# Kernel optimization log

Measured on AMD Instinct MI355X. Metric: run time of the kernel, lower is better.

## Reference

```python
import jax, jax.numpy as jnp
import numpy as np

B, S, DIM, HD = 4, 1024, 2048, 128
H = DIM // HD  # 16 heads
GN_EPS = 1e-3  # Keras GroupNormalization default epsilon


def setup_inputs() -> dict:
    key = jax.random.key(0)
    ks = jax.random.split(key, 8)
    x = jax.random.normal(ks[0], (B, S, DIM), dtype=jnp.float32)
    k = jax.random.normal(ks[1], (B, S, DIM), dtype=jnp.float32)
    v = jax.random.normal(ks[2], (B, S, DIM), dtype=jnp.float32)
    # One shared QKV projection weight per head (dict.fromkeys bug in source
    # makes Q, K, V use the SAME Dense layer). Keras Dense: y = x @ W, W:(in,out)
    Wh = jax.random.normal(ks[3], (H, HD, HD), dtype=jnp.float32) / np.sqrt(HD)
    wg_w = jax.random.normal(ks[4], (DIM, DIM), dtype=jnp.float32) / np.sqrt(DIM)
    wo_w = jax.random.normal(ks[5], (DIM, DIM), dtype=jnp.float32) / np.sqrt(DIM)
    gn_gamma = jnp.ones((DIM,), dtype=jnp.float32)
    gn_beta = jnp.zeros((DIM,), dtype=jnp.float32)
    return {"x": x, "k": k, "v": v, "Wh": Wh, "wg_w": wg_w, "wo_w": wo_w,
            "gn_gamma": gn_gamma, "gn_beta": gn_beta}


def _decay_masks(n_heads, seq_len):
    # Source: band_part(gamma**(i-j), 0, -1) then transpose ->
    # D[h, i, j] = gamma_h ** (j - i) for j <= i, else 0.
    gam = 1.0 - 2.0 ** (-5.0 - jnp.arange(n_heads, dtype=jnp.float32))  # (H,)
    idx = jnp.arange(seq_len, dtype=jnp.float32)
    expo = idx[None, :] - idx[:, None]               # (S,S): j - i
    D = jnp.where(expo[None, :, :] <= 0,
                  gam[:, None, None] ** expo[None, :, :], 0.0)  # (H,S,S)
    # TF: D /= reduce_sum(D, 1)**0.5 broadcasts row-sums along the COLUMN axis
    return D / jnp.sqrt(D.sum(axis=-1))[:, None, :]


def reference(x, k, v, Wh, wg_w, wo_w, gn_gamma, gn_beta):
    b, s, dim = x.shape
    h, hd, _ = Wh.shape
    # split last axis into contiguous per-head chunks
    xh = x.reshape(b, s, h, hd)
    kh = k.reshape(b, s, h, hd)
    vh = v.reshape(b, s, h, hd)
    # Q, K, V share the same per-head weight (faithful to dict.fromkeys)
    Q = jnp.einsum('bshd,hde->bshe', xh, Wh)
    K = jnp.einsum('bshd,hde->bshe', kh, Wh)
    V = jnp.einsum('bshd,hde->bshe', vh, Wh)
    scores = jnp.einsum('bshe,bthe->bhst', Q, K) / jnp.sqrt(jnp.float32(hd))
    Dn = _decay_masks(h, s)                          # (H,S,S)
    masked = scores * Dn[None, :, :, :]              # (B,H,S,S)
    # source reduces over axis 0 == BATCH, then abs, then clamp at 1
    A = jnp.maximum(jnp.abs(masked.sum(axis=0)), 1.0)  # (H,S,S)
    O = jnp.einsum('hst,bthe->bshe', A, V).reshape(b, s, dim)
    # GroupNormalization(groups=1): per-token layernorm over channels
    mu = O.mean(axis=-1, keepdims=True)
    var = O.var(axis=-1, keepdims=True)
    Y = (O - mu) / jnp.sqrt(var + GN_EPS) * gn_gamma + gn_beta
    W = jax.nn.relu(x @ wg_w)                        # gated branch
    return (W * Y) @ wo_w
```

## Files before the change

kernel.cpp:

```cpp
#include <hip/hip_runtime.h>
#include <math.h>

constexpr int Bc = 4, Sc = 1024, Dc = 2048, HDc = 128, Hc = 16;
constexpr int BSc = Bc * Sc;
constexpr int KQKc = Bc * HDc;
#define GN_EPS 1e-3f

typedef __bf16 bf16x8 __attribute__((ext_vector_type(8)));
typedef __bf16 bf16x4 __attribute__((ext_vector_type(4)));
typedef float f32x4 __attribute__((ext_vector_type(4)));

constexpr size_t OFF_Q   = 0;
constexpr size_t OFF_K   = OFF_Q + (size_t)Hc * Sc * KQKc / 2;
constexpr size_t OFF_VB  = OFF_K + (size_t)Hc * Sc * KQKc / 2;
constexpr size_t OFF_VT  = OFF_VB + (size_t)BSc * Dc / 2;
constexpr size_t OFF_A   = OFF_VT + (size_t)BSc * Dc / 2;
constexpr size_t OFF_O   = OFF_A + (size_t)Hc * Sc * Sc / 2;
constexpr size_t OFF_CT  = OFF_O + (size_t)BSc * Dc;
constexpr size_t OFF_PN  = OFF_CT + (size_t)Hc * Sc;
constexpr size_t OFF_XB  = OFF_PN + (size_t)Hc * Sc;
constexpr size_t OFF_WGT = OFF_XB + (size_t)BSc * Dc / 2;
constexpr size_t OFF_WOT = OFF_WGT + (size_t)Dc * Dc / 2;
constexpr size_t OFF_SUF = OFF_WOT + (size_t)Dc * Dc / 2;
constexpr size_t OFF_T   = OFF_SUF + (size_t)64 * 9 * HDc;
constexpr size_t OFF_WHT = OFF_T + (size_t)64 * 8 * HDc;
constexpr size_t OFF_KB2 = OFF_A;
constexpr size_t OFF_VB2 = OFF_A + (size_t)BSc * Dc / 2;

#define GLOAD_LDS16(gp, lp)                                               \
  __builtin_amdgcn_global_load_lds(                                       \
      (const __attribute__((address_space(1))) void*)(gp),                \
      (__attribute__((address_space(3))) void*)(lp), 16, 0, 0)


__global__ __launch_bounds__(256) void k_tables(float* __restrict__ ct,
                                                float* __restrict__ pn) {
  int idx = blockIdx.x * 256 + threadIdx.x;
  int h = idx >> 10, t = idx & 1023;
  double gamma = 1.0 - exp2(-(double)(5 + h));
  double l2g = log2(gamma);
  double r = 1.0 / gamma;
  double rowsum = (exp2(-(double)(t + 1) * l2g) - 1.0) / (r - 1.0);
  ct[idx] = (float)(exp2((double)t * l2g) / sqrt(rowsum));
  pn[idx] = (float)exp2(-(double)t * l2g);
}

__global__ __launch_bounds__(256) void k_cast83(const float* __restrict__ s0,
                                                const float* __restrict__ s1,
                                                const float* __restrict__ s2,
                                                __bf16* __restrict__ d0,
                                                __bf16* __restrict__ d1,
                                                __bf16* __restrict__ d2) {
  const int y = blockIdx.y;
  const float* src = (y == 0) ? s0 : (y == 1) ? s1 : s2;
  __bf16* dst = (y == 0) ? d0 : (y == 1) ? d1 : d2;
  size_t i = ((size_t)blockIdx.x * 256 + threadIdx.x) * 8;
  float4 a = *(const float4*)(src + i);
  float4 b = *(const float4*)(src + i + 4);
  bf16x8 o;
  o[0] = (__bf16)a.x; o[1] = (__bf16)a.y; o[2] = (__bf16)a.z; o[3] = (__bf16)a.w;
  o[4] = (__bf16)b.x; o[5] = (__bf16)b.y; o[6] = (__bf16)b.z; o[7] = (__bf16)b.w;
  *(bf16x8*)(dst + i) = o;
}

__global__ __launch_bounds__(256) void k_castT(const float* __restrict__ src,
                                               __bf16* __restrict__ dst) {
  __shared__ float t[32][33];
  const int bx = blockIdx.x, by = blockIdx.y;
  const int tid = threadIdx.x;
  const int lx = tid & 31, ly = tid >> 5;
  #pragma unroll
  for (int r = 0; r < 32; r += 8)
    t[ly + r][lx] = src[(size_t)(by * 32 + ly + r) * Dc + bx * 32 + lx];
  __syncthreads();
  #pragma unroll
  for (int r = 0; r < 32; r += 8)
    dst[(size_t)(bx * 32 + ly + r) * Dc + by * 32 + lx] = (__bf16)t[lx][ly + r];
}

__global__ __launch_bounds__(256) void k_whT(const float* __restrict__ Wh,
                                             __bf16* __restrict__ WhT) {
  __shared__ float t[32][33];
  const int h = blockIdx.z;
  const int d0 = blockIdx.x * 32, e0 = blockIdx.y * 32;
  const int tid = threadIdx.x;
  const int lx = tid & 31, ly = tid >> 5;
  #pragma unroll
  for (int r = 0; r < 32; r += 8)
    t[ly + r][lx] = Wh[(size_t)h * HDc * HDc + (d0 + ly + r) * HDc + e0 + lx];
  __syncthreads();
  #pragma unroll
  for (int r = 0; r < 32; r += 8)
    WhT[(size_t)h * HDc * HDc + (e0 + ly + r) * HDc + d0 + lx] =
        (__bf16)t[lx][ly + r];
}

__global__ __launch_bounds__(512) void k_projm(const __bf16* __restrict__ Xb,
                                               const __bf16* __restrict__ Kb2,
                                               const __bf16* __restrict__ Vb2,
                                               const __bf16* __restrict__ WhT,
                                               __bf16* __restrict__ Qo,
                                               __bf16* __restrict__ Ko,
                                               __bf16* __restrict__ Vo) {
  const int r0 = blockIdx.x * 128;
  const int h = blockIdx.y;
  const int z = blockIdx.z;
  const __bf16* src = (z == 0) ? Xb : (z == 1) ? Kb2 : Vb2;
  __shared__ __bf16 As[128 * 32];
  __shared__ __bf16 Bs[128 * 32];
  const int tid = threadIdx.x;
  const int wave = tid >> 6, lane = tid & 63;
  const int wm = (wave >> 2) * 64, wn = (wave & 3) * 32;
  const int grow = wave * 16 + (lane >> 2);
  const int gkb = ((lane & 3) ^ ((lane >> 3) & 3)) * 8;
  const int rl = lane & 15, kq = lane >> 4;
  const int sw8 = (kq ^ ((rl >> 1) & 3)) * 8;
  const int cha = wm >> 4, chb = wn >> 4;
  const __bf16* wb = WhT + (size_t)h * HDc * HDc;
  f32x4 acc[4][2] = {{}};
  for (int k0 = 0; k0 < HDc; k0 += 32) {
    GLOAD_LDS16(src + (size_t)(r0 + grow) * Dc + h * HDc + k0 + gkb,
                As + wave * 512);
    GLOAD_LDS16(wb + (size_t)grow * HDc + k0 + gkb, Bs + wave * 512);
    __syncthreads();
    bf16x8 a[4], b[2];
    #pragma unroll
    for (int i = 0; i < 4; ++i)
      a[i] = *(const bf16x8*)&As[(cha + i) * 512 + rl * 32 + sw8];
    #pragma unroll
    for (int j = 0; j < 2; ++j)
      b[j] = *(const bf16x8*)&Bs[(chb + j) * 512 + rl * 32 + sw8];
    #pragma unroll
    for (int i = 0; i < 4; ++i)
      #pragma unroll
      for (int j = 0; j < 2; ++j)
        acc[i][j] = __builtin_amdgcn_mfma_f32_16x16x32_bf16(a[i], b[j],
                                                            acc[i][j], 0, 0, 0);
    __syncthreads();
  }
  #pragma unroll
  for (int i = 0; i < 4; ++i) {
    #pragma unroll
    for (int j = 0; j < 2; ++j) {
      const int col = wn + j * 16 + rl;
      #pragma unroll
      for (int r = 0; r < 4; ++r) {
        const int row = r0 + wm + i * 16 + kq * 4 + r;
        const __bf16 v = (__bf16)acc[i][j][r];
        if (z == 2) {
          Vo[(size_t)row * Dc + h * HDc + col] = v;
        } else {
          const int s = row & 1023, bb = row >> 10;
          __bf16* dst = (z == 0) ? Qo : Ko;
          dst[((size_t)(h * Sc + s) * Bc + bb) * HDc + col] = v;
        }
      }
    }
  }
}

__global__ __launch_bounds__(256) void k_vt(const __bf16* __restrict__ VB,
                                            __bf16* __restrict__ Vt) {
  __shared__ float tl[32][33];
  const int bh = blockIdx.z, bb = bh >> 4, h = bh & 15;
  const int t0 = blockIdx.x * 32, e0 = blockIdx.y * 32;
  const int tid = threadIdx.x;
  const int lx = tid & 31, ly = tid >> 5;
  #pragma unroll
  for (int r = 0; r < 32; r += 8)
    tl[ly + r][lx] =
        (float)VB[(size_t)(bb * Sc + t0 + ly + r) * Dc + h * HDc + e0 + lx];
  __syncthreads();
  #pragma unroll
  for (int r = 0; r < 32; r += 8)
    Vt[((size_t)bh * HDc + e0 + ly + r) * Sc + t0 + lx] = (__bf16)tl[lx][ly + r];
}

__global__ __launch_bounds__(256) void k_vsum(const __bf16* __restrict__ VB,
                                              float* __restrict__ T) {
  const int jj = blockIdx.x, bh = blockIdx.y;
  const int bb = bh >> 4, h = bh & 15;
  const int tid = threadIdx.x;
  const int tp = tid >> 7, e = tid & 127;
  const __bf16* base =
      VB + (size_t)(bb * Sc + jj * 128 + tp * 64) * Dc + h * HDc + e;
  float a0 = 0.f, a1 = 0.f, a2 = 0.f, a3 = 0.f;
  float a4 = 0.f, a5 = 0.f, a6 = 0.f, a7 = 0.f;
  for (int t = 0; t < 64; t += 8) {
    a0 += (float)base[(size_t)(t + 0) * Dc];
    a1 += (float)base[(size_t)(t + 1) * Dc];
    a2 += (float)base[(size_t)(t + 2) * Dc];
    a3 += (float)base[(size_t)(t + 3) * Dc];
    a4 += (float)base[(size_t)(t + 4) * Dc];
    a5 += (float)base[(size_t)(t + 5) * Dc];
    a6 += (float)base[(size_t)(t + 6) * Dc];
    a7 += (float)base[(size_t)(t + 7) * Dc];
  }
  const float s = ((a0 + a1) + (a2 + a3)) + ((a4 + a5) + (a6 + a7));
  __shared__ float red[2][128];
  red[tp][e] = s;
  __syncthreads();
  if (tp == 0)
    T[((size_t)bh * 8 + jj) * HDc + e] = red[0][e] + red[1][e];
}

__global__ __launch_bounds__(128) void k_vscan(const float* __restrict__ T,
                                               float* __restrict__ SufV) {
  const int bh = blockIdx.x;
  const int e = threadIdx.x;
  float acc = 0.f;
  SufV[((size_t)bh * 9 + 8) * HDc + e] = 0.f;
  for (int jj = 7; jj >= 1; --jj) {
    acc += T[((size_t)bh * 8 + jj) * HDc + e];
    SufV[((size_t)bh * 9 + jj) * HDc + e] = acc;
  }
}

__global__ __launch_bounds__(512) void k_ssm(const __bf16* __restrict__ Q,
                                             const __bf16* __restrict__ Kb,
                                             const float* __restrict__ ct,
                                             const float* __restrict__ pn,
                                             __bf16* __restrict__ A) {
  const int bx = blockIdx.x, by = blockIdx.y;
  if (bx > by) return;
  const int h = blockIdx.z;
  const int t0 = bx * 128, s0 = by * 128;
  const int tid = threadIdx.x;
  __bf16* Ah = A + (size_t)h * Sc * Sc;
  __shared__ __bf16 Qs[128 * 32];
  __shared__ __bf16 Ks[128 * 32];
  const int wave = tid >> 6, lane = tid & 63;
  const int wm = (wave >> 2) * 64, wn = (wave & 3) * 32;
  const int grow = wave * 16 + (lane >> 2);
  const int gkb = ((lane & 3) ^ ((lane >> 3) & 3)) * 8;
  const int rl = lane & 15, kq = lane >> 4;
  const int sw8 = (kq ^ ((rl >> 1) & 3)) * 8;
  const int cha = wm >> 4, chb = wn >> 4;
  f32x4 acc[4][2] = {{}};
  const __bf16* qbase = Q + (size_t)(h * Sc + s0) * KQKc;
  const __bf16* kbase = Kb + (size_t)(h * Sc + t0) * KQKc;
  for (int k0 = 0; k0 < KQKc; k0 += 32) {
    GLOAD_LDS16(qbase + (size_t)grow * KQKc + k0 + gkb, Qs + wave * 512);
    GLOAD_LDS16(kbase + (size_t)grow * KQKc + k0 + gkb, Ks + wave * 512);
    __syncthreads();
    bf16x8 a[4], b[2];
    #pragma unroll
    for (int i = 0; i < 4; ++i)
      a[i] = *(const bf16x8*)&Qs[(cha + i) * 512 + rl * 32 + sw8];
    #pragma unroll
    for (int j = 0; j < 2; ++j)
      b[j] = *(const bf16x8*)&Ks[(chb + j) * 512 + rl * 32 + sw8];
    #pragma unroll
    for (int i = 0; i < 4; ++i)
      #pragma unroll
      for (int j = 0; j < 2; ++j)
        acc[i][j] = __builtin_amdgcn_mfma_f32_16x16x32_bf16(a[i], b[j],
                                                            acc[i][j], 0, 0, 0);
    __syncthreads();
  }
  const float rs = 0.088388347648318447f;
  #pragma unroll
  for (int i = 0; i < 4; ++i) {
    #pragma unroll
    for (int j = 0; j < 2; ++j) {
      const int t = t0 + wn + j * 16 + rl;
      const float ctv = ct[h * Sc + t] * rs;
      #pragma unroll
      for (int r = 0; r < 4; ++r) {
        const int s = s0 + wm + i * 16 + kq * 4 + r;
        float v = 1.0f;
        if (t <= s) v = fmaxf(fabsf(ctv * pn[h * Sc + s] * acc[i][j][r]), 1.0f);
        Ah[(size_t)s * Sc + t] = (__bf16)v;
      }
    }
  }
}

__global__ __launch_bounds__(512) void k_avm(const __bf16* __restrict__ A,
                                             const __bf16* __restrict__ Vt,
                                             const float* __restrict__ SufV,
                                             float* __restrict__ O) {
  const int bh = blockIdx.z, bb = bh >> 4, h = bh & 15;
  const int itile = blockIdx.x;
  const int s0 = itile * 128;
  const int tid = threadIdx.x;
  __shared__ __bf16 As[128 * 32];
  __shared__ __bf16 Bs[128 * 32];
  const int wave = tid >> 6, lane = tid & 63;
  const int wm = (wave >> 2) * 64, wn = (wave & 3) * 32;
  const int grow = wave * 16 + (lane >> 2);
  const int gkb = ((lane & 3) ^ ((lane >> 3) & 3)) * 8;
  const int rl = lane & 15, kq = lane >> 4;
  const int sw8 = (kq ^ ((rl >> 1) & 3)) * 8;
  const int cha = wm >> 4, chb = wn >> 4;
  f32x4 acc[4][2] = {{}};
  const __bf16* abase = A + (size_t)(h * Sc + s0) * Sc;
  const __bf16* vbase = Vt + (size_t)bh * HDc * Sc;
  const int kmax = (itile + 1) * 128;
  for (int k0 = 0; k0 < kmax; k0 += 32) {
    GLOAD_LDS16(abase + (size_t)grow * Sc + k0 + gkb, As + wave * 512);
    GLOAD_LDS16(vbase + (size_t)grow * Sc + k0 + gkb, Bs + wave * 512);
    __syncthreads();
    bf16x8 a[4], b[2];
    #pragma unroll
    for (int i = 0; i < 4; ++i)
      a[i] = *(const bf16x8*)&As[(cha + i) * 512 + rl * 32 + sw8];
    #pragma unroll
    for (int j = 0; j < 2; ++j)
      b[j] = *(const bf16x8*)&Bs[(chb + j) * 512 + rl * 32 + sw8];
    #pragma unroll
    for (int i = 0; i < 4; ++i)
      #pragma unroll
      for (int j = 0; j < 2; ++j)
        acc[i][j] = __builtin_amdgcn_mfma_f32_16x16x32_bf16(a[i], b[j],
                                                            acc[i][j], 0, 0, 0);
    __syncthreads();
  }
  const float* sufr = SufV + ((size_t)bh * 9 + (itile + 1)) * HDc;
  #pragma unroll
  for (int i = 0; i < 4; ++i) {
    #pragma unroll
    for (int j = 0; j < 2; ++j) {
      const int e = wn + j * 16 + rl;
      const float sv = sufr[e];
      #pragma unroll
      for (int r = 0; r < 4; ++r) {
        const int s = s0 + wm + i * 16 + kq * 4 + r;
        O[(size_t)(bb * Sc + s) * Dc + h * HDc + e] = acc[i][j][r] + sv;
      }
    }
  }
}

__global__ __launch_bounds__(256) void k_gnorm(float* __restrict__ O,
                                               const float* __restrict__ gw,
                                               const float* __restrict__ bw) {
  const int r = blockIdx.x;
  const int tid = threadIdx.x;
  float* row = O + (size_t)r * Dc;
  const int c = tid * 4;
  float4 v0 = *(const float4*)(row + c);
  float4 v1 = *(const float4*)(row + c + 1024);
  __shared__ float red[256];
  __shared__ float sh_mu, sh_inv;
  red[tid] = v0.x + v0.y + v0.z + v0.w + v1.x + v1.y + v1.z + v1.w;
  __syncthreads();
  for (int st = 128; st > 0; st >>= 1) {
    if (tid < st) red[tid] += red[tid + st];
    __syncthreads();
  }
  if (tid == 0) sh_mu = red[0] * (1.0f / Dc);
  __syncthreads();
  const float mu = sh_mu;
  float d[8] = {v0.x - mu, v0.y - mu, v0.z - mu, v0.w - mu,
                v1.x - mu, v1.y - mu, v1.z - mu, v1.w - mu};
  float ssq = 0.f;
  #pragma unroll
  for (int i = 0; i < 8; ++i) ssq += d[i] * d[i];
  red[tid] = ssq;
  __syncthreads();
  for (int st = 128; st > 0; st >>= 1) {
    if (tid < st) red[tid] += red[tid + st];
    __syncthreads();
  }
  if (tid == 0) sh_inv = rsqrtf(red[0] * (1.0f / Dc) + GN_EPS);
  __syncthreads();
  const float inv = sh_inv;
  float4 g0 = *(const float4*)(gw + c), g1 = *(const float4*)(gw + c + 1024);
  float4 b0 = *(const float4*)(bw + c), b1 = *(const float4*)(bw + c + 1024);
  float4 o0, o1;
  o0.x = d[0] * inv * g0.x + b0.x; o0.y = d[1] * inv * g0.y + b0.y;
  o0.z = d[2] * inv * g0.z + b0.z; o0.w = d[3] * inv * g0.w + b0.w;
  o1.x = d[4] * inv * g1.x + b1.x; o1.y = d[5] * inv * g1.y + b1.y;
  o1.z = d[6] * inv * g1.z + b1.z; o1.w = d[7] * inv * g1.w + b1.w;
  *(float4*)(row + c) = o0;
  *(float4*)(row + c + 1024) = o1;
}

constexpr int NTK = Dc / 64;
constexpr int ABUFE = 128 * 64;
constexpr int BBUFE = 128 * 64;
constexpr int MG_LDS = (3 * ABUFE + 2 * BBUFE) * 2;

__global__ __launch_bounds__(256, 2) void k_mgemm(const __bf16* __restrict__ Ab,
                                                  const __bf16* __restrict__ Bt,
                                                  const float* __restrict__ Y,
                                                  __bf16* __restrict__ Gout,
                                                  float* __restrict__ Fout,
                                                  int mode) {
  extern __shared__ __bf16 lds[];
  __bf16* As = lds;
  __bf16* Bs = lds + 3 * ABUFE;
  int wid = blockIdx.y * gridDim.x + blockIdx.x;
  wid = (wid & 7) * 64 + (wid >> 3);
  const int r0 = (wid >> 4) * 128;
  const int c0 = (wid & 15) * 128;
  const int tid = threadIdx.x;
  const int wave = tid >> 6, lane = tid & 63;
  const int wr = wave >> 1, wc = wave & 1;
  const int lr = lane >> 2;
  const int lkx = ((lane & 3) ^ ((lane >> 3) & 3)) * 8;
  const int rl = lane & 15, kq = lane >> 4;
  const int swo = rl * 32 + ((kq ^ ((rl >> 1) & 3)) * 8);
  f32x4 acc[4][4] = {{}};

#define STAGE_A_(i, kt, bsel) do {                                          \
    const int ci_ = (i) * 4 + wave;                                         \
    GLOAD_LDS16(Ab + (size_t)(r0 + (ci_ >> 1) * 16 + lr) * Dc               \
                    + (kt) * 64 + (ci_ & 1) * 32 + lkx,                     \
                As + (bsel) * ABUFE + ci_ * 512);                           \
  } while (0)
#define STAGE_B_(j, kt, bsel) do {                                          \
    const int ci_ = (j) * 4 + wave;                                         \
    GLOAD_LDS16(Bt + (size_t)(c0 + (ci_ >> 1) * 16 + lr) * Dc               \
                    + (kt) * 64 + (ci_ & 1) * 32 + lkx,                     \
                Bs + (bsel) * BBUFE + ci_ * 512);                           \
  } while (0)

  STAGE_A_(0, 0, 0); STAGE_A_(1, 0, 0); STAGE_A_(2, 0, 0); STAGE_A_(3, 0, 0);
  STAGE_B_(0, 0, 0); STAGE_B_(1, 0, 0); STAGE_B_(2, 0, 0); STAGE_B_(3, 0, 0);
  STAGE_A_(0, 1, 1); STAGE_A_(1, 1, 1); STAGE_A_(2, 1, 1); STAGE_A_(3, 1, 1);
  __builtin_amdgcn_sched_barrier(0);
  asm volatile("s_waitcnt vmcnt(4)" ::: "memory");
  __builtin_amdgcn_sched_barrier(0);
  __builtin_amdgcn_s_barrier();

  int cbA = 0;
  for (int t = 0; t < NTK; ++t) {
    const int sbA = (cbA + 2 >= 3) ? cbA - 1 : cbA + 2;
    const __bf16* Ac = As + cbA * ABUFE;
    const __bf16* Bc = Bs + (t & 1) * BBUFE;
    bf16x8 a[4][2], b[4][2];
    #pragma unroll
    for (int m = 0; m < 2; ++m)
      #pragma unroll
      for (int kc = 0; kc < 2; ++kc)
        a[m][kc] = *(const bf16x8*)&Ac[((wr * 4 + m) * 2 + kc) * 512 + swo];
    #pragma unroll
    for (int n = 0; n < 2; ++n)
      #pragma unroll
      for (int kc = 0; kc < 2; ++kc)
        b[n][kc] = *(const bf16x8*)&Bc[((wc * 4 + n) * 2 + kc) * 512 + swo];
    #pragma unroll
    for (int m = 2; m < 4; ++m)
      #pragma unroll
      for (int kc = 0; kc < 2; ++kc)
        a[m][kc] = *(const bf16x8*)&Ac[((wr * 4 + m) * 2 + kc) * 512 + swo];
    #pragma unroll
    for (int n = 2; n < 4; ++n)
      #pragma unroll
      for (int kc = 0; kc < 2; ++kc)
        b[n][kc] = *(const bf16x8*)&Bc[((wc * 4 + n) * 2 + kc) * 512 + swo];
    if (t + 1 < NTK) {
      STAGE_B_(0, t + 1, (t + 1) & 1); STAGE_B_(1, t + 1, (t + 1) & 1);
      STAGE_B_(2, t + 1, (t + 1) & 1); STAGE_B_(3, t + 1, (t + 1) & 1);
    }
    if (t + 2 < NTK) {
      STAGE_A_(0, t + 2, sbA); STAGE_A_(1, t + 2, sbA);
      STAGE_A_(2, t + 2, sbA); STAGE_A_(3, t + 2, sbA);
    }
    __builtin_amdgcn_sched_barrier(0);
    __builtin_amdgcn_s_setprio(1);
    #pragma unroll
    for (int kc = 0; kc < 2; ++kc)
      #pragma unroll
      for (int m = 0; m < 2; ++m)
        #pragma unroll
        for (int n = 0; n < 2; ++n)
          acc[m][n] = __builtin_amdgcn_mfma_f32_16x16x32_bf16(
              a[m][kc], b[n][kc], acc[m][n], 0, 0, 0);
    __builtin_amdgcn_s_setprio(0);
    __builtin_amdgcn_sched_barrier(0);
    __builtin_amdgcn_s_setprio(1);
    #pragma unroll
    for (int kc = 0; kc < 2; ++kc)
      #pragma unroll
      for (int m = 2; m < 4; ++m)
        #pragma unroll
        for (int n = 0; n < 2; ++n)
          acc[m][n] = __builtin_amdgcn_mfma_f32_16x16x32_bf16(
              a[m][kc], b[n][kc], acc[m][n], 0, 0, 0);
    __builtin_amdgcn_s_setprio(0);
    __builtin_amdgcn_sched_barrier(0);
    __builtin_amdgcn_s_setprio(1);
    #pragma unroll
    for (int kc = 0; kc < 2; ++kc)
      #pragma unroll
      for (int m = 0; m < 2; ++m)
        #pragma unroll
        for (int n = 2; n < 4; ++n)
          acc[m][n] = __builtin_amdgcn_mfma_f32_16x16x32_bf16(
              a[m][kc], b[n][kc], acc[m][n], 0, 0, 0);
    __builtin_amdgcn_s_setprio(0);
    __builtin_amdgcn_sched_barrier(0);
    __builtin_amdgcn_s_setprio(1);
    #pragma unroll
    for (int kc = 0; kc < 2; ++kc)
      #pragma unroll
      for (int m = 2; m < 4; ++m)
        #pragma unroll
        for (int n = 2; n < 4; ++n)
          acc[m][n] = __builtin_amdgcn_mfma_f32_16x16x32_bf16(
              a[m][kc], b[n][kc], acc[m][n], 0, 0, 0);
    __builtin_amdgcn_s_setprio(0);
    __builtin_amdgcn_sched_barrier(0);
    asm volatile("s_waitcnt lgkmcnt(0)" ::: "memory");
    __builtin_amdgcn_sched_barrier(0);
    if (t + 2 < NTK)
      asm volatile("s_waitcnt vmcnt(4)" ::: "memory");
    else if (t + 1 < NTK)
      asm volatile("s_waitcnt vmcnt(0)" ::: "memory");
    __builtin_amdgcn_sched_barrier(0);
    __builtin_amdgcn_s_barrier();
    cbA = (cbA + 1 >= 3) ? 0 : cbA + 1;
  }
#undef STAGE_A_
#undef STAGE_B_

  #pragma unroll
  for (int mi = 0; mi < 4; ++mi) {
    #pragma unroll
    for (int nj = 0; nj < 4; ++nj) {
      const int col = c0 + wc * 64 + nj * 16 + rl;
      #pragma unroll
      for (int r = 0; r < 4; ++r) {
        const int row = r0 + wr * 64 + mi * 16 + kq * 4 + r;
        const size_t idx = (size_t)row * Dc + col;
        float v = acc[mi][nj][r];
        if (mode == 0) {
          v = fmaxf(v, 0.f) * Y[idx];
          Gout[idx] = (__bf16)v;
        } else {
          Fout[idx] = v;
        }
      }
    }
  }
}

extern "C" void kernel_launch(void* const* d_in, const int* in_sizes, int n_in,
                              void* d_out, int out_size, void* d_ws, size_t ws_size,
                              hipStream_t stream) {
  const float* x  = (const float*)d_in[0];
  const float* k  = (const float*)d_in[1];
  const float* v  = (const float*)d_in[2];
  const float* Wh = (const float*)d_in[3];
  const float* wg = (const float*)d_in[4];
  const float* wo = (const float*)d_in[5];
  const float* gg = (const float*)d_in[6];
  const float* gb = (const float*)d_in[7];
  float* ws = (float*)d_ws;
  __bf16* Q   = (__bf16*)(ws + OFF_Q);
  __bf16* Kp  = (__bf16*)(ws + OFF_K);
  __bf16* VB  = (__bf16*)(ws + OFF_VB);
  __bf16* Vt  = (__bf16*)(ws + OFF_VT);
  __bf16* A   = (__bf16*)(ws + OFF_A);
  float*  O   = ws + OFF_O;
  float*  CT  = ws + OFF_CT;
  float*  PN  = ws + OFF_PN;
  __bf16* XB  = (__bf16*)(ws + OFF_XB);
  __bf16* WGT = (__bf16*)(ws + OFF_WGT);
  __bf16* WOT = (__bf16*)(ws + OFF_WOT);
  float*  SUF = ws + OFF_SUF;
  float*  TP  = ws + OFF_T;
  __bf16* WHT = (__bf16*)(ws + OFF_WHT);
  __bf16* KB2 = (__bf16*)(ws + OFF_KB2);
  __bf16* VB2 = (__bf16*)(ws + OFF_VB2);
  __bf16* G   = (__bf16*)(ws + OFF_Q);

  static bool attr_done = false;
  if (!attr_done) {
    (void)hipFuncSetAttribute((const void*)k_mgemm,
                              hipFuncAttributeMaxDynamicSharedMemorySize,
                              MG_LDS);
    attr_done = true;
  }

  k_tables<<<Hc * Sc / 256, 256, 0, stream>>>(CT, PN);
  k_cast83<<<dim3((BSc * Dc) / (256 * 8), 3), 256, 0, stream>>>(
      x, k, v, XB, KB2, VB2);
  k_castT<<<dim3(Dc / 32, Dc / 32), 256, 0, stream>>>(wg, WGT);
  k_castT<<<dim3(Dc / 32, Dc / 32), 256, 0, stream>>>(wo, WOT);
  k_whT<<<dim3(4, 4, Hc), 256, 0, stream>>>(Wh, WHT);
  k_projm<<<dim3(BSc / 128, Hc, 3), 512, 0, stream>>>(XB, KB2, VB2, WHT,
                                                      Q, Kp, VB);
  k_vt<<<dim3(Sc / 32, HDc / 32, Bc * Hc), 256, 0, stream>>>(VB, Vt);
  k_vsum<<<dim3(8, Bc * Hc), 256, 0, stream>>>(VB, TP);
  k_vscan<<<Bc * Hc, 128, 0, stream>>>(TP, SUF);
  k_ssm<<<dim3(Sc / 128, Sc / 128, Hc), 512, 0, stream>>>(Q, Kp, CT, PN, A);
  k_avm<<<dim3(Sc / 128, 1, Bc * Hc), 512, 0, stream>>>(A, Vt, SUF, O);
  k_gnorm<<<BSc, 256, 0, stream>>>(O, gg, gb);
  k_mgemm<<<dim3(16, 32), 256, MG_LDS, stream>>>(XB, WGT, O, G, nullptr, 0);
  k_mgemm<<<dim3(16, 32), 256, MG_LDS, stream>>>(G, WOT, nullptr, nullptr,
                                                 (float*)d_out, 1);
}
```

Before: 379.6 us.

## Share pipelined 128x128 MFMA mainloop across projection, score and AV kernels

Pulls the triple/double-buffered, software-pipelined MFMA loop out of the gate/output GEMM into a reusable template. The QKV projection, masked score and A·V kernels now use it in place of their simple single-buffered loops that synced twice per k-step. Those kernels drop from 512 to 256 threads, with each wave owning a 64x64 tile. Global-to-LDS loads now overlap MFMA work, at the cost of more dynamic LDS per block and possibly lower occupancy.

```diff
diff --git a/kernel.cpp b/kernel.cpp
--- a/kernel.cpp
+++ b/kernel.cpp
@@ -33,6 +33,137 @@
       (__attribute__((address_space(3))) void*)(lp), 16, 0, 0)
 
 
+constexpr int ABUFE = 128 * 64;
+constexpr int BBUFE = 128 * 64;
+constexpr int MG_LDS = (3 * ABUFE + 2 * BBUFE) * 2;
+
+template <int ASTR, int BSTR>
+__device__ __forceinline__ void mfma_loop128(const __bf16* __restrict__ Abase,
+                                             const __bf16* __restrict__ Bbase,
+                                             const int ntk,
+                                             __bf16* As, __bf16* Bs,
+                                             const int wave, const int lane,
+                                             f32x4 acc[4][4]) {
+  const int wr = wave >> 1, wc = wave & 1;
+  const int lr = lane >> 2;
+  const int lkx = ((lane & 3) ^ ((lane >> 3) & 3)) * 8;
+  const int rl = lane & 15, kq = lane >> 4;
+  const int swo = rl * 32 + ((kq ^ ((rl >> 1) & 3)) * 8);
+
+#define SA_(i, kt, bsel) do {                                               \
+    const int ci_ = (i) * 4 + wave;                                         \
+    GLOAD_LDS16(Abase + (size_t)((ci_ >> 1) * 16 + lr) * ASTR               \
+                    + (kt) * 64 + (ci_ & 1) * 32 + lkx,                     \
+                As + (bsel) * ABUFE + ci_ * 512);                           \
+  } while (0)
+#define SB_(j, kt, bsel) do {                                               \
+    const int ci_ = (j) * 4 + wave;                                         \
+    GLOAD_LDS16(Bbase + (size_t)((ci_ >> 1) * 16 + lr) * BSTR               \
+                    + (kt) * 64 + (ci_ & 1) * 32 + lkx,                     \
+                Bs + (bsel) * BBUFE + ci_ * 512);                           \
+  } while (0)
+
+  SA_(0, 0, 0); SA_(1, 0, 0); SA_(2, 0, 0); SA_(3, 0, 0);
+  SB_(0, 0, 0); SB_(1, 0, 0); SB_(2, 0, 0); SB_(3, 0, 0);
+  SA_(0, 1, 1); SA_(1, 1, 1); SA_(2, 1, 1); SA_(3, 1, 1);
+  __builtin_amdgcn_sched_barrier(0);
+  asm volatile("s_waitcnt vmcnt(4)" ::: "memory");
+  __builtin_amdgcn_sched_barrier(0);
+  __builtin_amdgcn_s_barrier();
+
+  int cbA = 0;
+  for (int t = 0; t < ntk; ++t) {
+    const int sbA = (cbA + 2 >= 3) ? cbA - 1 : cbA + 2;
+    const __bf16* Ac = As + cbA * ABUFE;
+    const __bf16* Bc = Bs + (t & 1) * BBUFE;
+    bf16x8 a[4][2], b[4][2];
+    #pragma unroll
+    for (int m = 0; m < 2; ++m)
+      #pragma unroll
+      for (int kc = 0; kc < 2; ++kc)
+        a[m][kc] = *(const bf16x8*)&Ac[((wr * 4 + m) * 2 + kc) * 512 + swo];
+    #pragma unroll
+    for (int n = 0; n < 2; ++n)
+      #pragma unroll
+      for (int kc = 0; kc < 2; ++kc)
+        b[n][kc] = *(const bf16x8*)&Bc[((wc * 4 + n) * 2 + kc) * 512 + swo];
+    #pragma unroll
+    for (int m = 2; m < 4; ++m)
+      #pragma unroll
+      for (int kc = 0; kc < 2; ++kc)
+        a[m][kc] = *(const bf16x8*)&Ac[((wr * 4 + m) * 2 + kc) * 512 + swo];
+    #pragma unroll
+    for (int n = 2; n < 4; ++n)
+      #pragma unroll
+      for (int kc = 0; kc < 2; ++kc)
+        b[n][kc] = *(const bf16x8*)&Bc[((wc * 4 + n) * 2 + kc) * 512 + swo];
+    if (t + 1 < ntk) {
+      SB_(0, t + 1, (t + 1) & 1); SB_(1, t + 1, (t + 1) & 1);
+      SB_(2, t + 1, (t + 1) & 1); SB_(3, t + 1, (t + 1) & 1);
+    }
+    if (t + 2 < ntk) {
+      SA_(0, t + 2, sbA); SA_(1, t + 2, sbA);
+      SA_(2, t + 2, sbA); SA_(3, t + 2, sbA);
+    }
+    __builtin_amdgcn_sched_barrier(0);
+    __builtin_amdgcn_s_setprio(1);
+    #pragma unroll
+    for (int kc = 0; kc < 2; ++kc)
+      #pragma unroll
+      for (int m = 0; m < 2; ++m)
+        #pragma unroll
+        for (int n = 0; n < 2; ++n)
+          acc[m][n] = __builtin_amdgcn_mfma_f32_16x16x32_bf16(
+              a[m][kc], b[n][kc], acc[m][n], 0, 0, 0);
+    __builtin_amdgcn_s_setprio(0);
+    __builtin_amdgcn_sched_barrier(0);
+    __builtin_amdgcn_s_setprio(1);
+    #pragma unroll
+    for (int kc = 0; kc < 2; ++kc)
+      #pragma unroll
+      for (int m = 2; m < 4; ++m)
+        #pragma unroll
+        for (int n = 0; n < 2; ++n)
+          acc[m][n] = __builtin_amdgcn_mfma_f32_16x16x32_bf16(
+              a[m][kc], b[n][kc], acc[m][n], 0, 0, 0);
+    __builtin_amdgcn_s_setprio(0);
+    __builtin_amdgcn_sched_barrier(0);
+    __builtin_amdgcn_s_setprio(1);
+    #pragma unroll
+    for (int kc = 0; kc < 2; ++kc)
+      #pragma unroll
+      for (int m = 0; m < 2; ++m)
+        #pragma unroll
+        for (int n = 2; n < 4; ++n)
+          acc[m][n] = __builtin_amdgcn_mfma_f32_16x16x32_bf16(
+              a[m][kc], b[n][kc], acc[m][n], 0, 0, 0);
+    __builtin_amdgcn_s_setprio(0);
+    __builtin_amdgcn_sched_barrier(0);
+    __builtin_amdgcn_s_setprio(1);
+    #pragma unroll
+    for (int kc = 0; kc < 2; ++kc)
+      #pragma unroll
+      for (int m = 2; m < 4; ++m)
+        #pragma unroll
+        for (int n = 2; n < 4; ++n)
+          acc[m][n] = __builtin_amdgcn_mfma_f32_16x16x32_bf16(
+              a[m][kc], b[n][kc], acc[m][n], 0, 0, 0);
+    __builtin_amdgcn_s_setprio(0);
+    __builtin_amdgcn_sched_barrier(0);
+    asm volatile("s_waitcnt lgkmcnt(0)" ::: "memory");
+    __builtin_amdgcn_sched_barrier(0);
+    if (t + 2 < ntk)
+      asm volatile("s_waitcnt vmcnt(4)" ::: "memory");
+    else if (t + 1 < ntk)
+      asm volatile("s_waitcnt vmcnt(0)" ::: "memory");
+    __builtin_amdgcn_sched_barrier(0);
+    __builtin_amdgcn_s_barrier();
+    cbA = (cbA + 1 >= 3) ? 0 : cbA + 1;
+  }
+#undef SA_
+#undef SB_
+}
+
 __global__ __launch_bounds__(256) void k_tables(float* __restrict__ ct,
                                                 float* __restrict__ pn) {
   int idx = blockIdx.x * 256 + threadIdx.x;
@@ -95,58 +226,37 @@
         (__bf16)t[lx][ly + r];
 }
 
-__global__ __launch_bounds__(512) void k_projm(const __bf16* __restrict__ Xb,
-                                               const __bf16* __restrict__ Kb2,
-                                               const __bf16* __restrict__ Vb2,
-                                               const __bf16* __restrict__ WhT,
-                                               __bf16* __restrict__ Qo,
-                                               __bf16* __restrict__ Ko,
-                                               __bf16* __restrict__ Vo) {
+__global__ __launch_bounds__(256, 2) void k_projm(const __bf16* __restrict__ Xb,
+                                                  const __bf16* __restrict__ Kb2,
+                                                  const __bf16* __restrict__ Vb2,
+                                                  const __bf16* __restrict__ WhT,
+                                                  __bf16* __restrict__ Qo,
+                                                  __bf16* __restrict__ Ko,
+                                                  __bf16* __restrict__ Vo) {
+  extern __shared__ __bf16 lds[];
+  __bf16* As = lds;
+  __bf16* Bs = lds + 3 * ABUFE;
   const int r0 = blockIdx.x * 128;
   const int h = blockIdx.y;
   const int z = blockIdx.z;
   const __bf16* src = (z == 0) ? Xb : (z == 1) ? Kb2 : Vb2;
-  __shared__ __bf16 As[128 * 32];
-  __shared__ __bf16 Bs[128 * 32];
   const int tid = threadIdx.x;
   const int wave = tid >> 6, lane = tid & 63;
-  const int wm = (wave >> 2) * 64, wn = (wave & 3) * 32;
-  const int grow = wave * 16 + (lane >> 2);
-  const int gkb = ((lane & 3) ^ ((lane >> 3) & 3)) * 8;
+  f32x4 acc[4][4] = {{}};
+  mfma_loop128<Dc, HDc>(src + (size_t)r0 * Dc + h * HDc,
+                        WhT + (size_t)h * HDc * HDc, 2, As, Bs, wave, lane,
+                        acc);
+  const int wr = wave >> 1, wc = wave & 1;
   const int rl = lane & 15, kq = lane >> 4;
-  const int sw8 = (kq ^ ((rl >> 1) & 3)) * 8;
-  const int cha = wm >> 4, chb = wn >> 4;
-  const __bf16* wb = WhT + (size_t)h * HDc * HDc;
-  f32x4 acc[4][2] = {{}};
-  for (int k0 = 0; k0 < HDc; k0 += 32) {
-    GLOAD_LDS16(src + (size_t)(r0 + grow) * Dc + h * HDc + k0 + gkb,
-                As + wave * 512);
-    GLOAD_LDS16(wb + (size_t)grow * HDc + k0 + gkb, Bs + wave * 512);
-    __syncthreads();
-    bf16x8 a[4], b[2];
-    #pragma unroll
-    for (int i = 0; i < 4; ++i)
-      a[i] = *(const bf16x8*)&As[(cha + i) * 512 + rl * 32 + sw8];
-    #pragma unroll
-    for (int j = 0; j < 2; ++j)
-      b[j] = *(const bf16x8*)&Bs[(chb + j) * 512 + rl * 32 + sw8];
-    #pragma unroll
-    for (int i = 0; i < 4; ++i)
-      #pragma unroll
-      for (int j = 0; j < 2; ++j)
-        acc[i][j] = __builtin_amdgcn_mfma_f32_16x16x32_bf16(a[i], b[j],
-                                                            acc[i][j], 0, 0, 0);
-    __syncthreads();
-  }
-  #pragma unroll
-  for (int i = 0; i < 4; ++i) {
-    #pragma unroll
-    for (int j = 0; j < 2; ++j) {
-      const int col = wn + j * 16 + rl;
+  #pragma unroll
+  for (int mi = 0; mi < 4; ++mi) {
+    #pragma unroll
+    for (int nj = 0; nj < 4; ++nj) {
+      const int col = wc * 64 + nj * 16 + rl;
       #pragma unroll
       for (int r = 0; r < 4; ++r) {
-        const int row = r0 + wm + i * 16 + kq * 4 + r;
-        const __bf16 v = (__bf16)acc[i][j][r];
+        const int row = r0 + wr * 64 + mi * 16 + kq * 4 + r;
+        const __bf16 v = (__bf16)acc[mi][nj][r];
         if (z == 2) {
           Vo[(size_t)row * Dc + h * HDc + col] = v;
         } else {
@@ -216,117 +326,74 @@
   }
 }
 
-__global__ __launch_bounds__(512) void k_ssm(const __bf16* __restrict__ Q,
-                                             const __bf16* __restrict__ Kb,
-                                             const float* __restrict__ ct,
-                                             const float* __restrict__ pn,
-                                             __bf16* __restrict__ A) {
+__global__ __launch_bounds__(256, 2) void k_ssm(const __bf16* __restrict__ Q,
+                                                const __bf16* __restrict__ Kb,
+                                                const float* __restrict__ ct,
+                                                const float* __restrict__ pn,
+                                                __bf16* __restrict__ A) {
   const int bx = blockIdx.x, by = blockIdx.y;
   if (bx > by) return;
+  extern __shared__ __bf16 lds[];
+  __bf16* As = lds;
+  __bf16* Bs = lds + 3 * ABUFE;
   const int h = blockIdx.z;
   const int t0 = bx * 128, s0 = by * 128;
   const int tid = threadIdx.x;
   __bf16* Ah = A + (size_t)h * Sc * Sc;
-  __shared__ __bf16 Qs[128 * 32];
-  __shared__ __bf16 Ks[128 * 32];
   const int wave = tid >> 6, lane = tid & 63;
-  const int wm = (wave >> 2) * 64, wn = (wave & 3) * 32;
-  const int grow = wave * 16 + (lane >> 2);
-  const int gkb = ((lane & 3) ^ ((lane >> 3) & 3)) * 8;
+  f32x4 acc[4][4] = {{}};
+  mfma_loop128<KQKc, KQKc>(Q + (size_t)(h * Sc + s0) * KQKc,
+                           Kb + (size_t)(h * Sc + t0) * KQKc, KQKc / 64, As,
+                           Bs, wave, lane, acc);
+  const int wr = wave >> 1, wc = wave & 1;
   const int rl = lane & 15, kq = lane >> 4;
-  const int sw8 = (kq ^ ((rl >> 1) & 3)) * 8;
-  const int cha = wm >> 4, chb = wn >> 4;
-  f32x4 acc[4][2] = {{}};
-  const __bf16* qbase = Q + (size_t)(h * Sc + s0) * KQKc;
-  const __bf16* kbase = Kb + (size_t)(h * Sc + t0) * KQKc;
-  for (int k0 = 0; k0 < KQKc; k0 += 32) {
-    GLOAD_LDS16(qbase + (size_t)grow * KQKc + k0 + gkb, Qs + wave * 512);
-    GLOAD_LDS16(kbase + (size_t)grow * KQKc + k0 + gkb, Ks + wave * 512);
-    __syncthreads();
-    bf16x8 a[4], b[2];
-    #pragma unroll
-    for (int i = 0; i < 4; ++i)
-      a[i] = *(const bf16x8*)&Qs[(cha + i) * 512 + rl * 32 + sw8];
-    #pragma unroll
-    for (int j = 0; j < 2; ++j)
-      b[j] = *(const bf16x8*)&Ks[(chb + j) * 512 + rl * 32 + sw8];
-    #pragma unroll
-    for (int i = 0; i < 4; ++i)
-      #pragma unroll
-      for (int j = 0; j < 2; ++j)
-        acc[i][j] = __builtin_amdgcn_mfma_f32_16x16x32_bf16(a[i], b[j],
-                                                            acc[i][j], 0, 0, 0);
-    __syncthreads();
-  }
   const float rs = 0.088388347648318447f;
   #pragma unroll
-  for (int i = 0; i < 4; ++i) {
-    #pragma unroll
-    for (int j = 0; j < 2; ++j) {
-      const int t = t0 + wn + j * 16 + rl;
+  for (int mi = 0; mi < 4; ++mi) {
+    #pragma unroll
+    for (int nj = 0; nj < 4; ++nj) {
+      const int t = t0 + wc * 64 + nj * 16 + rl;
       const float ctv = ct[h * Sc + t] * rs;
       #pragma unroll
       for (int r = 0; r < 4; ++r) {
-        const int s = s0 + wm + i * 16 + kq * 4 + r;
+        const int s = s0 + wr * 64 + mi * 16 + kq * 4 + r;
         float v = 1.0f;
-        if (t <= s) v = fmaxf(fabsf(ctv * pn[h * Sc + s] * acc[i][j][r]), 1.0f);
+        if (t <= s) v = fmaxf(fabsf(ctv * pn[h * Sc + s] * acc[mi][nj][r]), 1.0f);
         Ah[(size_t)s * Sc + t] = (__bf16)v;
       }
     }
   }
 }
 
-__global__ __launch_bounds__(512) void k_avm(const __bf16* __restrict__ A,
-                                             const __bf16* __restrict__ Vt,
-                                             const float* __restrict__ SufV,
-                                             float* __restrict__ O) {
+__global__ __launch_bounds__(256, 2) void k_avm(const __bf16* __restrict__ A,
+                                                const __bf16* __restrict__ Vt,
+                                                const float* __restrict__ SufV,
+                                                float* __restrict__ O) {
+  extern __shared__ __bf16 lds[];
+  __bf16* As = lds;
+  __bf16* Bs = lds + 3 * ABUFE;
   const int bh = blockIdx.z, bb = bh >> 4, h = bh & 15;
   const int itile = blockIdx.x;
   const int s0 = itile * 128;
   const int tid = threadIdx.x;
-  __shared__ __bf16 As[128 * 32];
-  __shared__ __bf16 Bs[128 * 32];
   const int wave = tid >> 6, lane = tid & 63;
-  const int wm = (wave >> 2) * 64, wn = (wave & 3) * 32;
-  const int grow = wave * 16 + (lane >> 2);
-  const int gkb = ((lane & 3) ^ ((lane >> 3) & 3)) * 8;
+  f32x4 acc[4][4] = {{}};
+  mfma_loop128<Sc, Sc>(A + (size_t)(h * Sc + s0) * Sc,
+                       Vt + (size_t)bh * HDc * Sc, (itile + 1) * 2, As, Bs,
+                       wave, lane, acc);
+  const int wr = wave >> 1, wc = wave & 1;
   const int rl = lane & 15, kq = lane >> 4;
-  const int sw8 = (kq ^ ((rl >> 1) & 3)) * 8;
-  const int cha = wm >> 4, chb = wn >> 4;
-  f32x4 acc[4][2] = {{}};
-  const __bf16* abase = A + (size_t)(h * Sc + s0) * Sc;
-  const __bf16* vbase = Vt + (size_t)bh * HDc * Sc;
-  const int kmax = (itile + 1) * 128;
-  for (int k0 = 0; k0 < kmax; k0 += 32) {
-    GLOAD_LDS16(abase + (size_t)grow * Sc + k0 + gkb, As + wave * 512);
-    GLOAD_LDS16(vbase + (size_t)grow * Sc + k0 + gkb, Bs + wave * 512);
-    __syncthreads();
-    bf16x8 a[4], b[2];
-    #pragma unroll
-    for (int i = 0; i < 4; ++i)
-      a[i] = *(const bf16x8*)&As[(cha + i) * 512 + rl * 32 + sw8];
-    #pragma unroll
-    for (int j = 0; j < 2; ++j)
-      b[j] = *(const bf16x8*)&Bs[(chb + j) * 512 + rl * 32 + sw8];
-    #pragma unroll
-    for (int i = 0; i < 4; ++i)
-      #pragma unroll
-      for (int j = 0; j < 2; ++j)
-        acc[i][j] = __builtin_amdgcn_mfma_f32_16x16x32_bf16(a[i], b[j],
-                                                            acc[i][j], 0, 0, 0);
-    __syncthreads();
-  }
   const float* sufr = SufV + ((size_t)bh * 9 + (itile + 1)) * HDc;
   #pragma unroll
-  for (int i = 0; i < 4; ++i) {
-    #pragma unroll
-    for (int j = 0; j < 2; ++j) {
-      const int e = wn + j * 16 + rl;
+  for (int mi = 0; mi < 4; ++mi) {
+    #pragma unroll
+    for (int nj = 0; nj < 4; ++nj) {
+      const int e = wc * 64 + nj * 16 + rl;
       const float sv = sufr[e];
       #pragma unroll
       for (int r = 0; r < 4; ++r) {
-        const int s = s0 + wm + i * 16 + kq * 4 + r;
-        O[(size_t)(bb * Sc + s) * Dc + h * HDc + e] = acc[i][j][r] + sv;
+        const int s = s0 + wr * 64 + mi * 16 + kq * 4 + r;
+        O[(size_t)(bb * Sc + s) * Dc + h * HDc + e] = acc[mi][nj][r] + sv;
       }
     }
   }
@@ -376,11 +443,6 @@
   *(float4*)(row + c) = o0;
   *(float4*)(row + c + 1024) = o1;
 }
-
-constexpr int NTK = Dc / 64;
-constexpr int ABUFE = 128 * 64;
-constexpr int BBUFE = 128 * 64;
-constexpr int MG_LDS = (3 * ABUFE + 2 * BBUFE) * 2;
 
 __global__ __launch_bounds__(256, 2) void k_mgemm(const __bf16* __restrict__ Ab,
                                                   const __bf16* __restrict__ Bt,
@@ -397,126 +459,11 @@
   const int c0 = (wid & 15) * 128;
   const int tid = threadIdx.x;
   const int wave = tid >> 6, lane = tid & 63;
+  f32x4 acc[4][4] = {{}};
+  mfma_loop128<Dc, Dc>(Ab + (size_t)r0 * Dc, Bt + (size_t)c0 * Dc, Dc / 64,
+                       As, Bs, wave, lane, acc);
   const int wr = wave >> 1, wc = wave & 1;
-  const int lr = lane >> 2;
-  const int lkx = ((lane & 3) ^ ((lane >> 3) & 3)) * 8;
   const int rl = lane & 15, kq = lane >> 4;
-  const int swo = rl * 32 + ((kq ^ ((rl >> 1) & 3)) * 8);
-  f32x4 acc[4][4] = {{}};
-
-#define STAGE_A_(i, kt, bsel) do {                                          \
-    const int ci_ = (i) * 4 + wave;                                         \
-    GLOAD_LDS16(Ab + (size_t)(r0 + (ci_ >> 1) * 16 + lr) * Dc               \
-                    + (kt) * 64 + (ci_ & 1) * 32 + lkx,                     \
-                As + (bsel) * ABUFE + ci_ * 512);                           \
-  } while (0)
-#define STAGE_B_(j, kt, bsel) do {                                          \
-    const int ci_ = (j) * 4 + wave;                                         \
-    GLOAD_LDS16(Bt + (size_t)(c0 + (ci_ >> 1) * 16 + lr) * Dc               \
-                    + (kt) * 64 + (ci_ & 1) * 32 + lkx,                     \
-                Bs + (bsel) * BBUFE + ci_ * 512);                           \
-  } while (0)
-
-  STAGE_A_(0, 0, 0); STAGE_A_(1, 0, 0); STAGE_A_(2, 0, 0); STAGE_A_(3, 0, 0);
-  STAGE_B_(0, 0, 0); STAGE_B_(1, 0, 0); STAGE_B_(2, 0, 0); STAGE_B_(3, 0, 0);
-  STAGE_A_(0, 1, 1); STAGE_A_(1, 1, 1); STAGE_A_(2, 1, 1); STAGE_A_(3, 1, 1);
-  __builtin_amdgcn_sched_barrier(0);
-  asm volatile("s_waitcnt vmcnt(4)" ::: "memory");
-  __builtin_amdgcn_sched_barrier(0);
-  __builtin_amdgcn_s_barrier();
-
-  int cbA = 0;
-  for (int t = 0; t < NTK; ++t) {
-    const int sbA = (cbA + 2 >= 3) ? cbA - 1 : cbA + 2;
-    const __bf16* Ac = As + cbA * ABUFE;
-    const __bf16* Bc = Bs + (t & 1) * BBUFE;
-    bf16x8 a[4][2], b[4][2];
-    #pragma unroll
-    for (int m = 0; m < 2; ++m)
-      #pragma unroll
-      for (int kc = 0; kc < 2; ++kc)
-        a[m][kc] = *(const bf16x8*)&Ac[((wr * 4 + m) * 2 + kc) * 512 + swo];
-    #pragma unroll
-    for (int n = 0; n < 2; ++n)
-      #pragma unroll
-      for (int kc = 0; kc < 2; ++kc)
-        b[n][kc] = *(const bf16x8*)&Bc[((wc * 4 + n) * 2 + kc) * 512 + swo];
-    #pragma unroll
-    for (int m = 2; m < 4; ++m)
-      #pragma unroll
-      for (int kc = 0; kc < 2; ++kc)
-        a[m][kc] = *(const bf16x8*)&Ac[((wr * 4 + m) * 2 + kc) * 512 + swo];
-    #pragma unroll
-    for (int n = 2; n < 4; ++n)
-      #pragma unroll
-      for (int kc = 0; kc < 2; ++kc)
-        b[n][kc] = *(const bf16x8*)&Bc[((wc * 4 + n) * 2 + kc) * 512 + swo];
-    if (t + 1 < NTK) {
-      STAGE_B_(0, t + 1, (t + 1) & 1); STAGE_B_(1, t + 1, (t + 1) & 1);
-      STAGE_B_(2, t + 1, (t + 1) & 1); STAGE_B_(3, t + 1, (t + 1) & 1);
-    }
-    if (t + 2 < NTK) {
-      STAGE_A_(0, t + 2, sbA); STAGE_A_(1, t + 2, sbA);
-      STAGE_A_(2, t + 2, sbA); STAGE_A_(3, t + 2, sbA);
-    }
-    __builtin_amdgcn_sched_barrier(0);
-    __builtin_amdgcn_s_setprio(1);
-    #pragma unroll
-    for (int kc = 0; kc < 2; ++kc)
-      #pragma unroll
-      for (int m = 0; m < 2; ++m)
-        #pragma unroll
-        for (int n = 0; n < 2; ++n)
-          acc[m][n] = __builtin_amdgcn_mfma_f32_16x16x32_bf16(
-              a[m][kc], b[n][kc], acc[m][n], 0, 0, 0);
-    __builtin_amdgcn_s_setprio(0);
-    __builtin_amdgcn_sched_barrier(0);
-    __builtin_amdgcn_s_setprio(1);
-    #pragma unroll
-    for (int kc = 0; kc < 2; ++kc)
-      #pragma unroll
-      for (int m = 2; m < 4; ++m)
-        #pragma unroll
-        for (int n = 0; n < 2; ++n)
-          acc[m][n] = __builtin_amdgcn_mfma_f32_16x16x32_bf16(
-              a[m][kc], b[n][kc], acc[m][n], 0, 0, 0);
-    __builtin_amdgcn_s_setprio(0);
-    __builtin_amdgcn_sched_barrier(0);
-    __builtin_amdgcn_s_setprio(1);
-    #pragma unroll
-    for (int kc = 0; kc < 2; ++kc)
-      #pragma unroll
-      for (int m = 0; m < 2; ++m)
-        #pragma unroll
-        for (int n = 2; n < 4; ++n)
-          acc[m][n] = __builtin_amdgcn_mfma_f32_16x16x32_bf16(
-              a[m][kc], b[n][kc], acc[m][n], 0, 0, 0);
-    __builtin_amdgcn_s_setprio(0);
-    __builtin_amdgcn_sched_barrier(0);
-    __builtin_amdgcn_s_setprio(1);
-    #pragma unroll
-    for (int kc = 0; kc < 2; ++kc)
-      #pragma unroll
-      for (int m = 2; m < 4; ++m)
-        #pragma unroll
-        for (int n = 2; n < 4; ++n)
-          acc[m][n] = __builtin_amdgcn_mfma_f32_16x16x32_bf16(
-              a[m][kc], b[n][kc], acc[m][n], 0, 0, 0);
-    __builtin_amdgcn_s_setprio(0);
-    __builtin_amdgcn_sched_barrier(0);
-    asm volatile("s_waitcnt lgkmcnt(0)" ::: "memory");
-    __builtin_amdgcn_sched_barrier(0);
-    if (t + 2 < NTK)
-      asm volatile("s_waitcnt vmcnt(4)" ::: "memory");
-    else if (t + 1 < NTK)
-      asm volatile("s_waitcnt vmcnt(0)" ::: "memory");
-    __builtin_amdgcn_sched_barrier(0);
-    __builtin_amdgcn_s_barrier();
-    cbA = (cbA + 1 >= 3) ? 0 : cbA + 1;
-  }
-#undef STAGE_A_
-#undef STAGE_B_
-
   #pragma unroll
   for (int mi = 0; mi < 4; ++mi) {
     #pragma unroll
@@ -573,6 +520,15 @@
     (void)hipFuncSetAttribute((const void*)k_mgemm,
                               hipFuncAttributeMaxDynamicSharedMemorySize,
                               MG_LDS);
+    (void)hipFuncSetAttribute((const void*)k_projm,
+                              hipFuncAttributeMaxDynamicSharedMemorySize,
+                              MG_LDS);
+    (void)hipFuncSetAttribute((const void*)k_ssm,
+                              hipFuncAttributeMaxDynamicSharedMemorySize,
+                              MG_LDS);
+    (void)hipFuncSetAttribute((const void*)k_avm,
+                              hipFuncAttributeMaxDynamicSharedMemorySize,
+                              MG_LDS);
     attr_done = true;
   }
 
@@ -582,13 +538,14 @@
   k_castT<<<dim3(Dc / 32, Dc / 32), 256, 0, stream>>>(wg, WGT);
   k_castT<<<dim3(Dc / 32, Dc / 32), 256, 0, stream>>>(wo, WOT);
   k_whT<<<dim3(4, 4, Hc), 256, 0, stream>>>(Wh, WHT);
-  k_projm<<<dim3(BSc / 128, Hc, 3), 512, 0, stream>>>(XB, KB2, VB2, WHT,
-                                                      Q, Kp, VB);
+  k_projm<<<dim3(BSc / 128, Hc, 3), 256, MG_LDS, stream>>>(XB, KB2, VB2, WHT,
+                                                           Q, Kp, VB);
   k_vt<<<dim3(Sc / 32, HDc / 32, Bc * Hc), 256, 0, stream>>>(VB, Vt);
   k_vsum<<<dim3(8, Bc * Hc), 256, 0, stream>>>(VB, TP);
   k_vscan<<<Bc * Hc, 128, 0, stream>>>(TP, SUF);
-  k_ssm<<<dim3(Sc / 128, Sc / 128, Hc), 512, 0, stream>>>(Q, Kp, CT, PN, A);
-  k_avm<<<dim3(Sc / 128, 1, Bc * Hc), 512, 0, stream>>>(A, Vt, SUF, O);
+  k_ssm<<<dim3(Sc / 128, Sc / 128, Hc), 256, MG_LDS, stream>>>(Q, Kp, CT, PN,
+                                                               A);
+  k_avm<<<dim3(Sc / 128, 1, Bc * Hc), 256, MG_LDS, stream>>>(A, Vt, SUF, O);
   k_gnorm<<<BSc, 256, 0, stream>>>(O, gg, gb);
   k_mgemm<<<dim3(16, 32), 256, MG_LDS, stream>>>(XB, WGT, O, G, nullptr, 0);
   k_mgemm<<<dim3(16, 32), 256, MG_LDS, stream>>>(G, WOT, nullptr, nullptr,
```

Measured after the change: 376.1 us. Within noise of the previous version (-0.9%).
